# Performance work log

Measured on AMD Instinct MI355X. Metric: run time of the kernel, lower is better.

The kernel has to match this reference:

```python
import jax, jax.numpy as jnp
import numpy as np

B, L, D_OUT, D_HIDDEN = 16, 4096, 1024, 512
MAX_PHASE = 6.28
R_MIN, R_MAX = 0.9, 0.999


def setup_inputs() -> dict:
    key = jax.random.key(0)
    ks = jax.random.split(key, 8)
    x = jax.random.normal(ks[0], (B, L, D_OUT), dtype=jnp.float32)
    # theta_init: log(max_phase * u)
    u_th = jax.random.uniform(ks[1], (D_HIDDEN,), dtype=jnp.float32)
    theta_log = jnp.log(MAX_PHASE * u_th)
    # nu_init: log(-0.5 * log(u * (r_max^2 - r_min^2) + r_min^2))
    u_nu = jax.random.uniform(ks[2], (D_HIDDEN,), dtype=jnp.float32)
    nu_log = jnp.log(-0.5 * jnp.log(u_nu * (R_MAX**2 - R_MIN**2) + R_MIN**2))
    # gamma_log_init from (nu_log, theta_log)
    diag_lambda = jnp.exp(-jnp.exp(nu_log) + 1j * jnp.exp(theta_log))
    gamma_log = jnp.log(jnp.sqrt(1.0 - jnp.abs(diag_lambda) ** 2))
    b_norm = jnp.sqrt(2.0 * D_OUT)
    c_norm = jnp.sqrt(float(D_HIDDEN))
    B_re = jax.random.normal(ks[3], (D_HIDDEN, D_OUT), dtype=jnp.float32) / b_norm
    B_im = jax.random.normal(ks[4], (D_HIDDEN, D_OUT), dtype=jnp.float32) / b_norm
    C_re = jax.random.normal(ks[5], (D_OUT, D_HIDDEN), dtype=jnp.float32) / c_norm
    C_im = jax.random.normal(ks[6], (D_OUT, D_HIDDEN), dtype=jnp.float32) / c_norm
    D = jax.random.normal(ks[7], (D_OUT,), dtype=jnp.float32)
    return {"x": x, "theta_log": theta_log, "nu_log": nu_log, "gamma_log": gamma_log,
            "B_re": B_re, "B_im": B_im, "C_re": C_re, "C_im": C_im, "D": D}


def _binop(q_i, q_j):
    # associative op for linear recurrence h_t = A_t * h_{t-1} + b_t (diagonal A)
    A_i, b_i = q_i
    A_j, b_j = q_j
    return (A_j * A_i, A_j * b_i + b_j)


def reference(x, theta_log, nu_log, gamma_log, B_re, B_im, C_re, C_im, D):
    diag_lambda = jnp.exp(-jnp.exp(nu_log) + 1j * jnp.exp(theta_log))  # (H,)
    B_norm = (B_re + 1j * B_im) * jnp.exp(gamma_log)[:, None]          # (H, D)
    C = C_re + 1j * C_im                                               # (D, H)
    # input projection: Bu_t = B_norm @ x_t -> (B, L, H) complex
    Bu = jnp.einsum('hd,bld->blh', B_norm, x.astype(B_norm.dtype))
    Lam = jnp.broadcast_to(diag_lambda, Bu.shape)
    # parallel scan over the sequence axis
    _, h = jax.lax.associative_scan(_binop, (Lam, Bu), axis=1)         # (B, L, H)
    # readout: y_t = Re[C h_t] + D * x_t
    y = jnp.einsum('oh,blh->blo', C, h).real + D * x
    return (y, h[:, -1])
```

## Files before the change

kernel.cpp:

```cpp
#include <hip/hip_runtime.h>

#define NB 16
#define NL 4096
#define NDO 1024
#define NH 512
#define NM (NB*NL)
#define NK 1024
#define NN 1024
#define CH 128
#define NCHUNK (NL/CH)
#define YCOUNT ((size_t)NM*NDO)
#define HCOUNT ((size_t)NB*NH)

typedef unsigned short u16;
typedef float f32x4 __attribute__((ext_vector_type(4)));
typedef unsigned int u32x4 __attribute__((ext_vector_type(4)));
typedef __bf16 bf16x8 __attribute__((ext_vector_type(8)));

__device__ __forceinline__ u16 f2bf(float f){
  unsigned u = __float_as_uint(f);
  unsigned r = u + 0x7fffu + ((u >> 16) & 1u);
  return (u16)(r >> 16);
}
__device__ __forceinline__ float bf2f(u16 v){ return __uint_as_float(((unsigned)v) << 16); }
__device__ __forceinline__ unsigned pack2(float a, float b){
  return (unsigned)f2bf(a) | ((unsigned)f2bf(b) << 16);
}

__device__ __forceinline__ void gld_lds16(const u16* g, u16* l){
  __builtin_amdgcn_global_load_lds(
      (const __attribute__((address_space(1))) unsigned int*)g,
      (__attribute__((address_space(3))) unsigned int*)l,
      16, 0, 0);
}


__global__ void prep_w1(const float* __restrict__ Bre, const float* __restrict__ Bim,
                        const float* __restrict__ gl, u16* __restrict__ W1){
  int i = blockIdx.x * blockDim.x + threadIdx.x;
  if (i >= NH * NDO) return;
  int h = i / NDO, d = i % NDO;
  float g = expf(gl[h]);
  W1[(size_t)h * NK + d]        = f2bf(Bre[i] * g);
  W1[(size_t)(NH + h) * NK + d] = f2bf(Bim[i] * g);
}

__global__ void prep_w2(const float* __restrict__ Cre, const float* __restrict__ Cim,
                        u16* __restrict__ W2){
  int i = blockIdx.x * blockDim.x + threadIdx.x;
  if (i >= NDO * NH) return;
  int o = i / NH, k = i % NH;
  W2[(size_t)o * NK + k]      = f2bf(Cre[i]);
  W2[(size_t)o * NK + NH + k] = f2bf(-Cim[i]);
}

__global__ void prep_lam(const float* __restrict__ theta_log, const float* __restrict__ nu_log,
                         float* __restrict__ lam){
  int h = threadIdx.x;
  if (h >= NH) return;
  float nu = expf(nu_log[h]);
  float th = expf(theta_log[h]);
  float mag = expf(-nu);
  float lre = mag * cosf(th), lim = mag * sinf(th);
  double pre = (double)lre, pim = (double)lim;
  #pragma unroll
  for (int s = 0; s < 7; s++){
    double nr = pre*pre - pim*pim;
    double ni = 2.0*pre*pim;
    pre = nr; pim = ni;
  }
  lam[h]        = lre;
  lam[NH + h]   = lim;
  lam[2*NH + h] = (float)pre;
  lam[3*NH + h] = (float)pim;
}

__global__ __launch_bounds__(256) void convert_x(const float* __restrict__ X, u16* __restrict__ Xb){
  size_t i = ((size_t)blockIdx.x * 256 + threadIdx.x) * 8;
  f32x4 a = *(const f32x4*)(X + i);
  f32x4 b = *(const f32x4*)(X + i + 4);
  u32x4 p;
  p[0] = pack2(a[0], a[1]); p[1] = pack2(a[2], a[3]);
  p[2] = pack2(b[0], b[1]); p[3] = pack2(b[2], b[3]);
  *(u32x4*)(Xb + i) = p;
}

template<int MODE>
__global__ __launch_bounds__(256) void gemm_pipe3(const u16* __restrict__ A,
                                                  const u16* __restrict__ W,
                                                  const float* __restrict__ Xf,
                                                  const u16* __restrict__ Xh,
                                                  const float* __restrict__ Dv,
                                                  u16* __restrict__ outB,
                                                  float* __restrict__ outF){
  __shared__ __align__(16) u16 A0[128][32];
  __shared__ __align__(16) u16 B0[128][32];
  __shared__ __align__(16) u16 A1[128][32];
  __shared__ __align__(16) u16 B1[128][32];
  __shared__ __align__(16) u16 A2[128][32];
  __shared__ __align__(16) u16 B2[128][32];
  const int tid = threadIdx.x;
  const int bid = blockIdx.x;
  const int lid = (bid & 7) * 512 + (bid >> 3);
  const int m0 = (lid >> 3) << 7;
  const int n0 = (lid & 7) << 7;
  const int w = tid >> 6, lane = tid & 63;
  const int wm = w >> 1, wn = w & 1;

  const int sr = lane >> 2;
  const int sc = (lane & 3) << 3;
  const u16* ag = A + (size_t)(m0 + w*32 + sr) * NK + sc;
  const u16* bg = W + (size_t)(n0 + w*32 + sr) * NK + sc;

  f32x4 acc[4][4];
#pragma unroll
  for (int i = 0; i < 4; i++)
#pragma unroll
    for (int j = 0; j < 4; j++) acc[i][j] = (f32x4){0.f,0.f,0.f,0.f};

  const int klane = (lane >> 4) << 3;
  const int rowa = wm*64 + (lane & 15);
  const int rowb = wn*64 + (lane & 15);

#define STG(AT, BT, t) do {                                 \
    gld_lds16(ag + (t)*32,          &AT[w*32][0]);          \
    gld_lds16(ag + (t)*32 + 16*NK,  &AT[w*32+16][0]);       \
    gld_lds16(bg + (t)*32,          &BT[w*32][0]);          \
    gld_lds16(bg + (t)*32 + 16*NK,  &BT[w*32+16][0]);       \
  } while(0)
#define CMP(AT, BT) do {                                            \
    bf16x8 af[4], bv[4];                                            \
    _Pragma("unroll")                                               \
    for (int i = 0; i < 4; i++){                                    \
      af[i] = *(const bf16x8*)&AT[rowa + i*16][klane];              \
      bv[i] = *(const bf16x8*)&BT[rowb + i*16][klane];              \
    }                                                               \
    _Pragma("unroll")                                               \
    for (int i = 0; i < 4; i++)                                     \
      _Pragma("unroll")                                             \
      for (int j = 0; j < 4; j++)                                   \
        acc[i][j] = __builtin_amdgcn_mfma_f32_16x16x32_bf16(af[i], bv[j], acc[i][j], 0, 0, 0); \
  } while(0)
#define WVM(n)  asm volatile("s_waitcnt vmcnt(" #n ")" ::: "memory")
#define LGKM0() asm volatile("s_waitcnt lgkmcnt(0)" ::: "memory")
#define BAR()   asm volatile("s_barrier" ::: "memory")

  STG(A0, B0, 0);
  STG(A1, B1, 1);

  for (int t = 0; t < 30; t += 3) {
    STG(A2, B2, t + 2);
    WVM(8);
    BAR();
    CMP(A0, B0);
    LGKM0();
    BAR();
    STG(A0, B0, t + 3);
    WVM(8);
    BAR();
    CMP(A1, B1);
    LGKM0();
    BAR();
    STG(A1, B1, t + 4);
    WVM(8);
    BAR();
    CMP(A2, B2);
    LGKM0();
    BAR();
  }
  WVM(4);
  BAR();
  CMP(A0, B0);
  WVM(0);
  BAR();
  CMP(A1, B1);

#undef STG
#undef CMP
#undef WVM
#undef LGKM0
#undef BAR

  const int r0 = (lane >> 4) << 2;
  const int col = lane & 15;
#pragma unroll
  for (int i = 0; i < 4; i++){
    int gm = m0 + wm*64 + i*16 + r0;
#pragma unroll
    for (int j = 0; j < 4; j++){
      int gn = n0 + wn*64 + j*16 + col;
      if constexpr (MODE == 0) {
#pragma unroll
        for (int r = 0; r < 4; r++)
          outB[(size_t)(gm + r) * NN + gn] = f2bf(acc[i][j][r]);
      } else if constexpr (MODE == 1) {
        float dv = Dv[gn];
#pragma unroll
        for (int r = 0; r < 4; r++){
          size_t oidx = (size_t)(gm + r) * NDO + gn;
          outF[oidx] = acc[i][j][r] + dv * Xf[oidx];
        }
      } else {
        float dv = Dv[gn];
#pragma unroll
        for (int r = 0; r < 4; r++){
          size_t oidx = (size_t)(gm + r) * NDO + gn;
          outF[oidx] = acc[i][j][r] + dv * bf2f(Xh[oidx]);
        }
      }
    }
  }
}

template<int MODE>
__global__ __launch_bounds__(256) void gemm_pipe(const u16* __restrict__ A,
                                                 const u16* __restrict__ W,
                                                 const float* __restrict__ Xf,
                                                 const u16* __restrict__ Xh,
                                                 const float* __restrict__ Dv,
                                                 u16* __restrict__ outB,
                                                 float* __restrict__ outF){
  __shared__ __align__(16) u16 A0[128][32];
  __shared__ __align__(16) u16 B0[128][32];
  __shared__ __align__(16) u16 A1[128][32];
  __shared__ __align__(16) u16 B1[128][32];
  const int tid = threadIdx.x;
  const int bid = blockIdx.x;
  const int lid = (bid & 7) * 512 + (bid >> 3);
  const int m0 = (lid >> 3) << 7;
  const int n0 = (lid & 7) << 7;
  const int w = tid >> 6, lane = tid & 63;
  const int wm = w >> 1, wn = w & 1;

  const int sr = lane >> 2;
  const int sc = (lane & 3) << 3;
  const u16* ag = A + (size_t)(m0 + w*32 + sr) * NK + sc;
  const u16* bg = W + (size_t)(n0 + w*32 + sr) * NK + sc;

  f32x4 acc[4][4];
#pragma unroll
  for (int i = 0; i < 4; i++)
#pragma unroll
    for (int j = 0; j < 4; j++) acc[i][j] = (f32x4){0.f,0.f,0.f,0.f};

  const int klane = (lane >> 4) << 3;
  const int rowa = wm*64 + (lane & 15);
  const int rowb = wn*64 + (lane & 15);

#define STAGE0(k0) do {                               \
    gld_lds16(ag + (k0),          &A0[w*32][0]);      \
    gld_lds16(ag + (k0) + 16*NK,  &A0[w*32+16][0]);   \
    gld_lds16(bg + (k0),          &B0[w*32][0]);      \
    gld_lds16(bg + (k0) + 16*NK,  &B0[w*32+16][0]);   \
  } while(0)
#define STAGE1(k0) do {                               \
    gld_lds16(ag + (k0),          &A1[w*32][0]);      \
    gld_lds16(ag + (k0) + 16*NK,  &A1[w*32+16][0]);   \
    gld_lds16(bg + (k0),          &B1[w*32][0]);      \
    gld_lds16(bg + (k0) + 16*NK,  &B1[w*32+16][0]);   \
  } while(0)
#define COMPUTE(AT, BT) do {                                        \
    bf16x8 af[4], bv[4];                                            \
    _Pragma("unroll")                                               \
    for (int i = 0; i < 4; i++){                                    \
      af[i] = *(const bf16x8*)&AT[rowa + i*16][klane];              \
      bv[i] = *(const bf16x8*)&BT[rowb + i*16][klane];              \
    }                                                               \
    _Pragma("unroll")                                               \
    for (int i = 0; i < 4; i++)                                     \
      _Pragma("unroll")                                             \
      for (int j = 0; j < 4; j++)                                   \
        acc[i][j] = __builtin_amdgcn_mfma_f32_16x16x32_bf16(af[i], bv[j], acc[i][j], 0, 0, 0); \
  } while(0)
#define WAITVM(n) asm volatile("s_waitcnt vmcnt(" #n ")" ::: "memory")
#define LGKM0()   asm volatile("s_waitcnt lgkmcnt(0)" ::: "memory")
#define BAR()     asm volatile("s_barrier" ::: "memory")

  STAGE0(0);
  STAGE1(32);
  WAITVM(4);
  BAR();

  for (int k0 = 0; k0 < NK - 64; k0 += 64) {
    COMPUTE(A0, B0);
    LGKM0();
    BAR();
    STAGE0(k0 + 64);
    WAITVM(4);
    BAR();
    COMPUTE(A1, B1);
    LGKM0();
    BAR();
    STAGE1(k0 + 96);
    WAITVM(4);
    BAR();
  }
  COMPUTE(A0, B0);
  LGKM0();
  WAITVM(0);
  BAR();
  COMPUTE(A1, B1);

#undef STAGE0
#undef STAGE1
#undef COMPUTE
#undef WAITVM
#undef LGKM0
#undef BAR

  const int r0 = (lane >> 4) << 2;
  const int col = lane & 15;
#pragma unroll
  for (int i = 0; i < 4; i++){
    int gm = m0 + wm*64 + i*16 + r0;
#pragma unroll
    for (int j = 0; j < 4; j++){
      int gn = n0 + wn*64 + j*16 + col;
      if constexpr (MODE == 0) {
#pragma unroll
        for (int r = 0; r < 4; r++)
          outB[(size_t)(gm + r) * NN + gn] = f2bf(acc[i][j][r]);
      } else if constexpr (MODE == 1) {
        float dv = Dv[gn];
#pragma unroll
        for (int r = 0; r < 4; r++){
          size_t oidx = (size_t)(gm + r) * NDO + gn;
          outF[oidx] = acc[i][j][r] + dv * Xf[oidx];
        }
      } else {
        float dv = Dv[gn];
#pragma unroll
        for (int r = 0; r < 4; r++){
          size_t oidx = (size_t)(gm + r) * NDO + gn;
          outF[oidx] = acc[i][j][r] + dv * bf2f(Xh[oidx]);
        }
      }
    }
  }
}


__global__ __launch_bounds__(256) void gemm1_legacy(const float* __restrict__ X,
                                                    const u16* __restrict__ W1,
                                                    u16* __restrict__ Bu){
  __shared__ __align__(16) u16 Alds[128][32];
  __shared__ __align__(16) u16 Blds[128][32];
  const int tid = threadIdx.x;
  const int bid = blockIdx.x;
  const int lid = (bid & 7) * 512 + (bid >> 3);
  const int m0 = (lid >> 3) << 7;
  const int n0 = (lid & 7) << 7;
  const int w = tid >> 6, lane = tid & 63;
  const int wm = w >> 1, wn = w & 1;
  f32x4 acc[4][4];
#pragma unroll
  for (int i = 0; i < 4; i++)
#pragma unroll
    for (int j = 0; j < 4; j++) acc[i][j] = (f32x4){0.f,0.f,0.f,0.f};

  const int srow = tid >> 1;
  const int skseg = (tid & 1) << 4;
  const float* xp = X + (size_t)(m0 + srow) * NK + skseg;
  const u16*  wp  = W1 + (size_t)(n0 + srow) * NK + skseg;

  const int klane = (lane >> 4) << 3;
  const int rowa = wm*64 + (lane & 15);
  const int rowb = wn*64 + (lane & 15);

  for (int k0 = 0; k0 < NK; k0 += 32) {
    __syncthreads();
    f32x4 v0 = *(const f32x4*)(xp + k0 + 0);
    f32x4 v1 = *(const f32x4*)(xp + k0 + 4);
    f32x4 v2 = *(const f32x4*)(xp + k0 + 8);
    f32x4 v3 = *(const f32x4*)(xp + k0 + 12);
    u32x4 q0 = *(const u32x4*)(wp + k0);
    u32x4 q1 = *(const u32x4*)(wp + k0 + 8);
    u32x4 p0, p1;
    p0[0] = pack2(v0[0], v0[1]); p0[1] = pack2(v0[2], v0[3]);
    p0[2] = pack2(v1[0], v1[1]); p0[3] = pack2(v1[2], v1[3]);
    p1[0] = pack2(v2[0], v2[1]); p1[1] = pack2(v2[2], v2[3]);
    p1[2] = pack2(v3[0], v3[1]); p1[3] = pack2(v3[2], v3[3]);
    *(u32x4*)&Alds[srow][skseg]     = p0;
    *(u32x4*)&Alds[srow][skseg + 8] = p1;
    *(u32x4*)&Blds[srow][skseg]     = q0;
    *(u32x4*)&Blds[srow][skseg + 8] = q1;
    __syncthreads();
    bf16x8 af[4], bv[4];
#pragma unroll
    for (int i = 0; i < 4; i++){
      af[i] = *(const bf16x8*)&Alds[rowa + i*16][klane];
      bv[i] = *(const bf16x8*)&Blds[rowb + i*16][klane];
    }
#pragma unroll
    for (int i = 0; i < 4; i++)
#pragma unroll
      for (int j = 0; j < 4; j++)
        acc[i][j] = __builtin_amdgcn_mfma_f32_16x16x32_bf16(af[i], bv[j], acc[i][j], 0, 0, 0);
  }

  const int r0 = (lane >> 4) << 2;
  const int col = lane & 15;
#pragma unroll
  for (int i = 0; i < 4; i++){
    int gm = m0 + wm*64 + i*16 + r0;
#pragma unroll
    for (int j = 0; j < 4; j++){
      int gn = n0 + wn*64 + j*16 + col;
#pragma unroll
      for (int r = 0; r < 4; r++)
        Bu[(size_t)(gm + r) * NN + gn] = f2bf(acc[i][j][r]);
    }
  }
}


__global__ __launch_bounds__(512) void scan_carry(const u16* __restrict__ Bu,
                                                  const float* __restrict__ lam,
                                                  float* __restrict__ carry){
  const int h = threadIdx.x;
  const int bc = blockIdx.x;
  const int b = bc / NCHUNK, c = bc % NCHUNK;
  const float lre = lam[h], lim = lam[NH + h];
  float hre = 0.f, him = 0.f;
  size_t base = (size_t)(b * NL + c * CH) * NN;
  for (int j = 0; j < CH; j++){
    float bre = bf2f(Bu[base + (size_t)j*NN + h]);
    float bim = bf2f(Bu[base + (size_t)j*NN + NH + h]);
    float nre = lre*hre - lim*him + bre;
    float nim = lre*him + lim*hre + bim;
    hre = nre; him = nim;
  }
  size_t ci = ((size_t)bc * NH + h) * 2;
  carry[ci] = hre; carry[ci + 1] = him;
}

__global__ __launch_bounds__(512) void scan_combine(const float* __restrict__ carry,
                                                    const float* __restrict__ lam,
                                                    float* __restrict__ hstart){
  const int h = threadIdx.x;
  const int b = blockIdx.x;
  const float Pre = lam[2*NH + h], Pim = lam[3*NH + h];
  float are = 0.f, aim = 0.f;
  for (int c = 0; c < NCHUNK; c++){
    size_t idx = ((size_t)(b * NCHUNK + c) * NH + h) * 2;
    hstart[idx] = are; hstart[idx + 1] = aim;
    float cre = carry[idx], cim = carry[idx + 1];
    float nre = Pre*are - Pim*aim + cre;
    float nim = Pre*aim + Pim*are + cim;
    are = nre; aim = nim;
  }
}

__global__ __launch_bounds__(512) void scan_fixup(u16* __restrict__ Bu,
                                                  const float* __restrict__ lam,
                                                  const float* __restrict__ hstart,
                                                  float* __restrict__ out, int out_size){
  const int h = threadIdx.x;
  const int bc = blockIdx.x;
  const int b = bc / NCHUNK, c = bc % NCHUNK;
  const float lre = lam[h], lim = lam[NH + h];
  size_t si = ((size_t)bc * NH + h) * 2;
  const float sre = hstart[si], sim = hstart[si + 1];
  float hre = 0.f, him = 0.f;
  float pre = lre, pim = lim;
  size_t base = (size_t)(b * NL + c * CH) * NN;
  for (int j = 0; j < CH; j++){
    float bre = bf2f(Bu[base + (size_t)j*NN + h]);
    float bim = bf2f(Bu[base + (size_t)j*NN + NH + h]);
    float nre = lre*hre - lim*him + bre;
    float nim = lre*him + lim*hre + bim;
    hre = nre; him = nim;
    float vre = hre + pre*sre - pim*sim;
    float vim = him + pre*sim + pim*sre;
    Bu[base + (size_t)j*NN + h]      = f2bf(vre);
    Bu[base + (size_t)j*NN + NH + h] = f2bf(vim);
    if (c == NCHUNK - 1 && j == CH - 1){
      size_t ore_i = YCOUNT + (size_t)b * NH + h;
      size_t oim_i = YCOUNT + HCOUNT + (size_t)b * NH + h;
      if (ore_i < (size_t)out_size) out[ore_i] = vre;
      if (oim_i < (size_t)out_size) out[oim_i] = vim;
    }
    float qre = pre*lre - pim*lim;
    float qim = pre*lim + pim*lre;
    pre = qre; pim = qim;
  }
}


extern "C" void kernel_launch(void* const* d_in, const int* in_sizes, int n_in,
                              void* d_out, int out_size, void* d_ws, size_t ws_size,
                              hipStream_t stream) {
  const float* x         = (const float*)d_in[0];
  const float* theta_log = (const float*)d_in[1];
  const float* nu_log    = (const float*)d_in[2];
  const float* gamma_log = (const float*)d_in[3];
  const float* Bre       = (const float*)d_in[4];
  const float* Bim       = (const float*)d_in[5];
  const float* Cre       = (const float*)d_in[6];
  const float* Cim       = (const float*)d_in[7];
  const float* Dv        = (const float*)d_in[8];
  float* out = (float*)d_out;
  char* ws = (char*)d_ws;

  u16*   W1     = (u16*)(ws);
  u16*   W2     = (u16*)(ws + (2u << 20));
  float* lam    = (float*)(ws + (4u << 20));
  float* carry  = (float*)(ws + (5u << 20));
  float* hstart = (float*)(ws + (7u << 20));
  u16*   Bu     = (u16*)(ws + (16u << 20));
  u16*   Xb     = (u16*)(ws + (144u << 20));
  size_t need_base = (16u << 20) + (size_t)NM * NN * 2;
  size_t need_fast = need_base + (size_t)NM * NK * 2;
  if (ws_size < need_base) return;
  const bool fast = (ws_size >= need_fast);

  prep_w1<<<(NH * NDO + 255) / 256, 256, 0, stream>>>(Bre, Bim, gamma_log, W1);
  prep_w2<<<(NDO * NH + 255) / 256, 256, 0, stream>>>(Cre, Cim, W2);
  prep_lam<<<1, 512, 0, stream>>>(theta_log, nu_log, lam);

  if (fast) {
    convert_x<<<(int)(YCOUNT / (256*8)), 256, 0, stream>>>(x, Xb);
    gemm_pipe3<0><<<4096, 256, 0, stream>>>(Xb, W1, nullptr, nullptr, nullptr, Bu, nullptr);
  } else {
    gemm1_legacy<<<4096, 256, 0, stream>>>(x, W1, Bu);
  }

  scan_carry<<<NB * NCHUNK, 512, 0, stream>>>(Bu, lam, carry);
  scan_combine<<<NB, 512, 0, stream>>>(carry, lam, hstart);
  scan_fixup<<<NB * NCHUNK, 512, 0, stream>>>(Bu, lam, hstart, out, out_size);

  if (fast) {
    gemm_pipe<2><<<4096, 256, 0, stream>>>(Bu, W2, nullptr, Xb, Dv, nullptr, out);
  } else {
    gemm_pipe<1><<<4096, 256, 0, stream>>>(Bu, W2, x, nullptr, Dv, nullptr, out);
  }
}
```

Baseline: 611.7 us.

## Use BK=64 double-buffered GEMM with XOR-swizzled LDS for input projection

Replaces the triple-buffered K=32 tile pipeline of the first GEMM with a double-buffered K=64 tile. The LDS layout is XOR-swizzled so that the 16-byte fragment reads avoid bank conflicts. This halves the number of barrier and wait rounds per K step and doubles the MFMA work done between synchronisations. In exchange it drops to a shallower prefetch depth, which may expose more global-load latency.

New measurement: 580.0 us. -5.2%, faster.

```diff
diff --git a/kernel.cpp b/kernel.cpp
--- a/kernel.cpp
+++ b/kernel.cpp
@@ -86,19 +86,17 @@
 }
 
 template<int MODE>
-__global__ __launch_bounds__(256) void gemm_pipe3(const u16* __restrict__ A,
-                                                  const u16* __restrict__ W,
-                                                  const float* __restrict__ Xf,
-                                                  const u16* __restrict__ Xh,
-                                                  const float* __restrict__ Dv,
-                                                  u16* __restrict__ outB,
-                                                  float* __restrict__ outF){
-  __shared__ __align__(16) u16 A0[128][32];
-  __shared__ __align__(16) u16 B0[128][32];
-  __shared__ __align__(16) u16 A1[128][32];
-  __shared__ __align__(16) u16 B1[128][32];
-  __shared__ __align__(16) u16 A2[128][32];
-  __shared__ __align__(16) u16 B2[128][32];
+__global__ __launch_bounds__(256) void gemm_sz(const u16* __restrict__ A,
+                                               const u16* __restrict__ W,
+                                               const float* __restrict__ Xf,
+                                               const u16* __restrict__ Xh,
+                                               const float* __restrict__ Dv,
+                                               u16* __restrict__ outB,
+                                               float* __restrict__ outF){
+  __shared__ __align__(16) u16 A0[128][64];
+  __shared__ __align__(16) u16 B0[128][64];
+  __shared__ __align__(16) u16 A1[128][64];
+  __shared__ __align__(16) u16 B1[128][64];
   const int tid = threadIdx.x;
   const int bid = blockIdx.x;
   const int lid = (bid & 7) * 512 + (bid >> 3);
@@ -107,10 +105,10 @@
   const int w = tid >> 6, lane = tid & 63;
   const int wm = w >> 1, wn = w & 1;
 
-  const int sr = lane >> 2;
-  const int sc = (lane & 3) << 3;
-  const u16* ag = A + (size_t)(m0 + w*32 + sr) * NK + sc;
-  const u16* bg = W + (size_t)(n0 + w*32 + sr) * NK + sc;
+  const int grow = lane >> 3;
+  const int gcol = ((lane & 7) ^ grow) << 3;
+  const u16* Ag = A + (size_t)(m0 + w*32 + grow) * NK + gcol;
+  const u16* Bg = W + (size_t)(n0 + w*32 + grow) * NK + gcol;
 
   f32x4 acc[4][4];
 #pragma unroll
@@ -118,28 +116,38 @@
 #pragma unroll
     for (int j = 0; j < 4; j++) acc[i][j] = (f32x4){0.f,0.f,0.f,0.f};
 
-  const int klane = (lane >> 4) << 3;
-  const int rowa = wm*64 + (lane & 15);
-  const int rowb = wn*64 + (lane & 15);
-
-#define STG(AT, BT, t) do {                                 \
-    gld_lds16(ag + (t)*32,          &AT[w*32][0]);          \
-    gld_lds16(ag + (t)*32 + 16*NK,  &AT[w*32+16][0]);       \
-    gld_lds16(bg + (t)*32,          &BT[w*32][0]);          \
-    gld_lds16(bg + (t)*32 + 16*NK,  &BT[w*32+16][0]);       \
+  const int c15 = lane & 15;
+  const int q   = lane >> 4;
+  const int sw0 = ((q    ) ^ (lane & 7)) << 3;
+  const int sw1 = ((q | 4) ^ (lane & 7)) << 3;
+  const int rowa = wm*64 + c15;
+  const int rowb = wn*64 + c15;
+
+#define STG(AT, BT, t) do {                                      \
+    _Pragma("unroll")                                            \
+    for (int s = 0; s < 4; s++){                                 \
+      gld_lds16(Ag + (size_t)(t)*64 + (size_t)s*8*NK, &AT[w*32 + s*8][0]); \
+      gld_lds16(Bg + (size_t)(t)*64 + (size_t)s*8*NK, &BT[w*32 + s*8][0]); \
+    }                                                            \
   } while(0)
 #define CMP(AT, BT) do {                                            \
-    bf16x8 af[4], bv[4];                                            \
+    bf16x8 af[4][2], bv[4][2];                                      \
     _Pragma("unroll")                                               \
     for (int i = 0; i < 4; i++){                                    \
-      af[i] = *(const bf16x8*)&AT[rowa + i*16][klane];              \
-      bv[i] = *(const bf16x8*)&BT[rowb + i*16][klane];              \
+      const u16* pa = &AT[rowa + i*16][0];                          \
+      const u16* pb = &BT[rowb + i*16][0];                          \
+      af[i][0] = *(const bf16x8*)(pa + sw0);                        \
+      af[i][1] = *(const bf16x8*)(pa + sw1);                        \
+      bv[i][0] = *(const bf16x8*)(pb + sw0);                        \
+      bv[i][1] = *(const bf16x8*)(pb + sw1);                        \
     }                                                               \
     _Pragma("unroll")                                               \
     for (int i = 0; i < 4; i++)                                     \
       _Pragma("unroll")                                             \
-      for (int j = 0; j < 4; j++)                                   \
-        acc[i][j] = __builtin_amdgcn_mfma_f32_16x16x32_bf16(af[i], bv[j], acc[i][j], 0, 0, 0); \
+      for (int j = 0; j < 4; j++){                                  \
+        acc[i][j] = __builtin_amdgcn_mfma_f32_16x16x32_bf16(af[i][0], bv[j][0], acc[i][j], 0, 0, 0); \
+        acc[i][j] = __builtin_amdgcn_mfma_f32_16x16x32_bf16(af[i][1], bv[j][1], acc[i][j], 0, 0, 0); \
+      }                                                             \
   } while(0)
 #define WVM(n)  asm volatile("s_waitcnt vmcnt(" #n ")" ::: "memory")
 #define LGKM0() asm volatile("s_waitcnt lgkmcnt(0)" ::: "memory")
@@ -147,29 +155,23 @@
 
   STG(A0, B0, 0);
   STG(A1, B1, 1);
-
-  for (int t = 0; t < 30; t += 3) {
-    STG(A2, B2, t + 2);
-    WVM(8);
-    BAR();
+  WVM(8);
+  BAR();
+
+  for (int t = 0; t < 14; t += 2) {
     CMP(A0, B0);
     LGKM0();
     BAR();
-    STG(A0, B0, t + 3);
+    STG(A0, B0, t + 2);
     WVM(8);
     BAR();
     CMP(A1, B1);
     LGKM0();
     BAR();
-    STG(A1, B1, t + 4);
+    STG(A1, B1, t + 3);
     WVM(8);
     BAR();
-    CMP(A2, B2);
-    LGKM0();
-    BAR();
-  }
-  WVM(4);
-  BAR();
+  }
   CMP(A0, B0);
   WVM(0);
   BAR();
@@ -182,13 +184,12 @@
 #undef BAR
 
   const int r0 = (lane >> 4) << 2;
-  const int col = lane & 15;
 #pragma unroll
   for (int i = 0; i < 4; i++){
     int gm = m0 + wm*64 + i*16 + r0;
 #pragma unroll
     for (int j = 0; j < 4; j++){
-      int gn = n0 + wn*64 + j*16 + col;
+      int gn = n0 + wn*64 + j*16 + c15;
       if constexpr (MODE == 0) {
 #pragma unroll
         for (int r = 0; r < 4; r++)
@@ -520,7 +521,7 @@
 
   if (fast) {
     convert_x<<<(int)(YCOUNT / (256*8)), 256, 0, stream>>>(x, Xb);
-    gemm_pipe3<0><<<4096, 256, 0, stream>>>(Xb, W1, nullptr, nullptr, nullptr, Bu, nullptr);
+    gemm_sz<0><<<4096, 256, 0, stream>>>(Xb, W1, nullptr, nullptr, nullptr, Bu, nullptr);
   } else {
     gemm1_legacy<<<4096, 256, 0, stream>>>(x, W1, Bu);
   }
```
